# Optimization experiments

Measured on AMD Instinct MI355X. Metric: run time of the kernel, lower is better.

## Reference

```python
import jax, jax.numpy as jnp
import numpy as np

N_NODES = 50000

def setup_inputs() -> dict:
    key = jax.random.key(0)
    k1, k2, k3, k4, k5 = jax.random.split(key, 5)
    x = jax.random.normal(k1, (4, N_NODES, 128), dtype=jnp.float32)
    weights = jax.random.normal(k2, (128, 64), dtype=jnp.float32) * (np.sqrt(2.0) * np.sqrt(6.0 / (128 + 64)))
    edge_vals = jax.random.uniform(k3, (800000,), dtype=jnp.float32)
    edge_rows = jax.random.randint(k4, (800000,), 0, N_NODES, dtype=jnp.int32)
    edge_cols = jax.random.randint(k5, (800000,), 0, N_NODES, dtype=jnp.int32)
    return {"x": x, "weights": weights, "edge_vals": edge_vals,
            "edge_rows": edge_rows, "edge_cols": edge_cols}

def reference(x, weights, edge_vals, edge_rows, edge_cols):
    # x: [B, N, Din]; weights: [Din, Dout]; adj as COO edges (shared across batch)
    pre = jnp.einsum('bni,io->bno', x, weights)          # dense GEMM per sample
    msg = pre[:, edge_cols, :] * edge_vals[None, :, None]  # [B, E, Dout] gather+scale
    # sparse adj @ pre: scatter-add messages to destination rows, per batch sample
    agg = jax.vmap(lambda m: jax.ops.segment_sum(m, edge_rows, num_segments=N_NODES))(msg)
    return jax.nn.relu(agg)
```

## Files before the change

kernel.cpp:

```cpp
#include <hip/hip_runtime.h>
#include <hip/hip_bf16.h>


#define B_BATCH 4
#define DIN 128
#define DOUT 64
#define CAP 64

typedef float f32x4 __attribute__((ext_vector_type(4)));
typedef short s16x8 __attribute__((ext_vector_type(8)));

static __device__ __forceinline__ unsigned short f2bf(float f) {
  unsigned u = __builtin_bit_cast(unsigned, f);
  unsigned r = (u + 0x7fff + ((u >> 16) & 1)) >> 16;
  return (unsigned short)r;
}
static __device__ __forceinline__ float lo16(unsigned u) {
  return __builtin_bit_cast(float, u << 16);
}
static __device__ __forceinline__ float hi16(unsigned u) {
  return __builtin_bit_cast(float, u & 0xffff0000u);
}

__global__ __launch_bounds__(256) void prep_wfrag_zero_kernel(
    const float* __restrict__ w, uint4* __restrict__ wimg,
    int* __restrict__ cnt, int n) {
  const int t = threadIdx.x;
  if (blockIdx.x != 0) {
    int i = (blockIdx.x - 1) * 256 + t;
    if (i < n) cnt[i] = 0;
    return;
  }
  for (int i = 0; i < 8; ++i) {
    int idx = i * 256 + t;
    int fslot = idx >> 6;
    int lane = idx & 63;
    int term = fslot & 1;
    int cks = fslot >> 1;
    int ct = cks >> 2, ks = cks & 3;
    int nn = ct * 16 + (lane & 15);
    int kb = ks * 32 + 4 * ((lane >> 4) & 3);
    unsigned short e[8];
#pragma unroll
    for (int j = 0; j < 8; ++j) {
      int k = kb + 16 * (j >> 2) + (j & 3);
      float wv = w[k * DOUT + nn];
      unsigned ub = __builtin_bit_cast(unsigned, wv);
      unsigned hib = ub & 0xffff0000u;
      if (term == 0) {
        e[j] = (unsigned short)(hib >> 16);
      } else {
        float lof = wv - __builtin_bit_cast(float, hib);
        e[j] = (unsigned short)(__builtin_bit_cast(unsigned, lof) >> 16);
      }
    }
    uint4 q;
    q.x = (unsigned)e[0] | ((unsigned)e[1] << 16);
    q.y = (unsigned)e[2] | ((unsigned)e[3] << 16);
    q.z = (unsigned)e[4] | ((unsigned)e[5] << 16);
    q.w = (unsigned)e[6] | ((unsigned)e[7] << 16);
    wimg[idx] = q;
  }
}

__global__ __launch_bounds__(256) void gemm_fill_kernel(
    const float* __restrict__ x, const uint4* __restrict__ wimg,
    unsigned short* __restrict__ pre16, int N, int nWaveTiles,
    const int* __restrict__ erows, const int* __restrict__ ecols,
    const float* __restrict__ evals, int* __restrict__ cnt,
    int2* __restrict__ epk, int nE) {
  __shared__ uint4 wlds[2048];
  const int t = threadIdx.x;
  for (int i = t; i < 2048; i += 256) wlds[i] = wimg[i];
  __syncthreads();

  const int wtile = blockIdx.x * 4 + (t >> 6);
  if (wtile < nWaveTiles) {
    const int lane = t & 63;
    const int rowg = (lane >> 4) & 3;
    const int rloc = lane & 15;

    f32x4 acc[2][4];
#pragma unroll
    for (int rs = 0; rs < 2; ++rs)
#pragma unroll
      for (int ct = 0; ct < 4; ++ct) acc[rs][ct] = (f32x4){0.f, 0.f, 0.f, 0.f};

    const float* xb = x + (size_t)wtile * 32 * DIN;

#pragma unroll
    for (int ks = 0; ks < 4; ++ks) {
      s16x8 Ah[2], Al[2];
#pragma unroll
      for (int rs = 0; rs < 2; ++rs) {
        const float* xp = xb + (rs * 16 + rloc) * DIN + ks * 32 + 4 * rowg;
        float4 a0 = *(const float4*)xp;
        float4 a1 = *(const float4*)(xp + 16);

        unsigned b0 = __builtin_bit_cast(unsigned, a0.x);
        unsigned b1 = __builtin_bit_cast(unsigned, a0.y);
        unsigned b2 = __builtin_bit_cast(unsigned, a0.z);
        unsigned b3 = __builtin_bit_cast(unsigned, a0.w);
        unsigned c0 = __builtin_bit_cast(unsigned, a1.x);
        unsigned c1 = __builtin_bit_cast(unsigned, a1.y);
        unsigned c2 = __builtin_bit_cast(unsigned, a1.z);
        unsigned c3 = __builtin_bit_cast(unsigned, a1.w);

        union { s16x8 v; unsigned u[4]; } H, L;
        H.u[0] = (b0 >> 16) | (b1 & 0xffff0000u);
        H.u[1] = (b2 >> 16) | (b3 & 0xffff0000u);
        H.u[2] = (c0 >> 16) | (c1 & 0xffff0000u);
        H.u[3] = (c2 >> 16) | (c3 & 0xffff0000u);

        float l0 = a0.x - hi16(b0);
        float l1 = a0.y - hi16(b1);
        float l2 = a0.z - hi16(b2);
        float l3 = a0.w - hi16(b3);
        float l4 = a1.x - hi16(c0);
        float l5 = a1.y - hi16(c1);
        float l6 = a1.z - hi16(c2);
        float l7 = a1.w - hi16(c3);
        L.u[0] = (__builtin_bit_cast(unsigned, l0) >> 16) |
                 (__builtin_bit_cast(unsigned, l1) & 0xffff0000u);
        L.u[1] = (__builtin_bit_cast(unsigned, l2) >> 16) |
                 (__builtin_bit_cast(unsigned, l3) & 0xffff0000u);
        L.u[2] = (__builtin_bit_cast(unsigned, l4) >> 16) |
                 (__builtin_bit_cast(unsigned, l5) & 0xffff0000u);
        L.u[3] = (__builtin_bit_cast(unsigned, l6) >> 16) |
                 (__builtin_bit_cast(unsigned, l7) & 0xffff0000u);
        Ah[rs] = H.v;
        Al[rs] = L.v;
      }

#pragma unroll
      for (int ct = 0; ct < 4; ++ct) {
        const int fbase = (ct * 4 + ks) * 2;
        s16x8 Bh = *(const s16x8*)&wlds[fbase * 64 + lane];
        s16x8 Bl = *(const s16x8*)&wlds[(fbase + 1) * 64 + lane];
#pragma unroll
        for (int rs = 0; rs < 2; ++rs) {
          acc[rs][ct] = __builtin_amdgcn_mfma_f32_16x16x32_bf16(Ah[rs], Bh, acc[rs][ct], 0, 0, 0);
          acc[rs][ct] = __builtin_amdgcn_mfma_f32_16x16x32_bf16(Ah[rs], Bl, acc[rs][ct], 0, 0, 0);
          acc[rs][ct] = __builtin_amdgcn_mfma_f32_16x16x32_bf16(Al[rs], Bh, acc[rs][ct], 0, 0, 0);
        }
      }
    }

#pragma unroll
    for (int rs = 0; rs < 2; ++rs) {
#pragma unroll
      for (int r = 0; r < 4; ++r) {
        int m = wtile * 32 + rs * 16 + 4 * rowg + r;
        int b = m / N;
        int n = m - b * N;
        size_t o = (size_t)n * 256 + b * 64 + rloc;
#pragma unroll
        for (int ct = 0; ct < 4; ++ct) {
          pre16[o + ct * 16] = f2bf(acc[rs][ct][r]);
        }
      }
    }
  }

  const int stride = gridDim.x * 256;
  for (int e = blockIdx.x * 256 + t; e < nE; e += stride) {
    int r = erows[e];
    int slot = atomicAdd(&cnt[r], 1);
    if (slot < CAP)
      epk[r * CAP + slot] = make_int2(ecols[e], __builtin_bit_cast(int, evals[e]));
  }
}

__global__ __launch_bounds__(256) void gather_rows_kernel(
    const unsigned short* __restrict__ pre16, const int* __restrict__ cnt,
    const int2* __restrict__ epk, float* __restrict__ out, int N, int NS) {
  const int wid  = blockIdx.x * 4 + (threadIdx.x >> 6);
  const int lane = threadIdx.x & 63;
  if (wid >= N) return;

  const int m    = min(cnt[wid], CAP);
  const int eh   = lane >> 5;
  const int loff = ((lane >> 3) & 3) * 64 + (lane & 7) * 8;

  int   c = 0;
  float v = 0.0f;
  if (lane < m) {
    int2 r = epk[wid * CAP + lane];
    c = r.x;
    v = __builtin_bit_cast(float, r.y);
  }

  float a0 = 0.f, a1 = 0.f, a2 = 0.f, a3 = 0.f;
  float a4 = 0.f, a5 = 0.f, a6 = 0.f, a7 = 0.f;

  auto edge2 = [&](int j) {
    int   cj = __shfl(c, j + eh, 64);
    float vj = __shfl(v, j + eh, 64);
    const uint4 q = *(const uint4*)(pre16 + (size_t)cj * 256 + loff);
    a0 = fmaf(vj, lo16(q.x), a0);
    a1 = fmaf(vj, hi16(q.x), a1);
    a2 = fmaf(vj, lo16(q.y), a2);
    a3 = fmaf(vj, hi16(q.y), a3);
    a4 = fmaf(vj, lo16(q.z), a4);
    a5 = fmaf(vj, hi16(q.z), a5);
    a6 = fmaf(vj, lo16(q.w), a6);
    a7 = fmaf(vj, hi16(q.w), a7);
  };

  int j = 0;
  for (; j + 7 < m; j += 8) { edge2(j); edge2(j + 2); edge2(j + 4); edge2(j + 6); }
  for (; j + 1 < m; j += 2) { edge2(j); }
  if (j < m) {
    int   cj = __shfl(c, j, 64);
    float vj = __shfl(v, j, 64);
    if (eh) vj = 0.0f;
    const uint4 q = *(const uint4*)(pre16 + (size_t)cj * 256 + loff);
    a0 = fmaf(vj, lo16(q.x), a0);
    a1 = fmaf(vj, hi16(q.x), a1);
    a2 = fmaf(vj, lo16(q.y), a2);
    a3 = fmaf(vj, hi16(q.y), a3);
    a4 = fmaf(vj, lo16(q.z), a4);
    a5 = fmaf(vj, hi16(q.z), a5);
    a6 = fmaf(vj, lo16(q.w), a6);
    a7 = fmaf(vj, hi16(q.w), a7);
  }

  a0 += __shfl_xor(a0, 32, 64);
  a1 += __shfl_xor(a1, 32, 64);
  a2 += __shfl_xor(a2, 32, 64);
  a3 += __shfl_xor(a3, 32, 64);
  a4 += __shfl_xor(a4, 32, 64);
  a5 += __shfl_xor(a5, 32, 64);
  a6 += __shfl_xor(a6, 32, 64);
  a7 += __shfl_xor(a7, 32, 64);

  if (lane < 32) {
    const int b   = lane >> 3;
    const int ch8 = (lane & 7) * 8;
    size_t o = (size_t)b * NS + (size_t)wid * DOUT + ch8;
    *(float4*)&out[o]     = make_float4(fmaxf(a0, 0.f), fmaxf(a1, 0.f),
                                        fmaxf(a2, 0.f), fmaxf(a3, 0.f));
    *(float4*)&out[o + 4] = make_float4(fmaxf(a4, 0.f), fmaxf(a5, 0.f),
                                        fmaxf(a6, 0.f), fmaxf(a7, 0.f));
  }
}

extern "C" void kernel_launch(void* const* d_in, const int* in_sizes, int n_in,
                              void* d_out, int out_size, void* d_ws, size_t ws_size,
                              hipStream_t stream) {
  const float* x     = (const float*)d_in[0];
  const float* w     = (const float*)d_in[1];
  const float* evals = (const float*)d_in[2];
  const int*   erows = (const int*)d_in[3];
  const int*   ecols = (const int*)d_in[4];
  float* out = (float*)d_out;

  const int N  = in_sizes[0] / (B_BATCH * DIN);
  const int E  = in_sizes[2];
  const int M  = B_BATCH * N;
  const int NS = N * DOUT;
  const int nWaveTiles = M / 32;

  size_t off = 0;
  auto alloc = [&](size_t bytes) {
    size_t o = off;
    off += (bytes + 255) & ~(size_t)255;
    return o;
  };
  size_t pre_off  = alloc((size_t)M * DOUT * 2);
  size_t wimg_off = alloc((size_t)2048 * 16);
  size_t cnt_off  = alloc((size_t)N * 4);
  size_t epk_off  = alloc((size_t)N * CAP * 8);
  (void)ws_size;

  char* ws = (char*)d_ws;
  unsigned short* pre16 = (unsigned short*)(ws + pre_off);
  uint4* wimg = (uint4*)(ws + wimg_off);
  int*   cnt  = (int*)(ws + cnt_off);
  int2*  epk  = (int2*)(ws + epk_off);

  prep_wfrag_zero_kernel<<<1 + (N + 255) / 256, 256, 0, stream>>>(w, wimg, cnt, N);

  gemm_fill_kernel<<<(nWaveTiles + 3) / 4, 256, 0, stream>>>(
      x, wimg, pre16, N, nWaveTiles, erows, ecols, evals, cnt, epk, E);

  gather_rows_kernel<<<(N + 3) / 4, 256, 0, stream>>>(pre16, cnt, epk, out, N, NS);
}
```

Baseline: 130.4 us.

## Split edge bucketing out of GEMM kernel and prefetch next x k-slice

```diff
diff --git a/kernel.cpp b/kernel.cpp
--- a/kernel.cpp
+++ b/kernel.cpp
@@ -63,112 +63,128 @@
   }
 }
 
-__global__ __launch_bounds__(256) void gemm_fill_kernel(
+__global__ __launch_bounds__(256, 4) void gemm_mfma_kernel(
     const float* __restrict__ x, const uint4* __restrict__ wimg,
-    unsigned short* __restrict__ pre16, int N, int nWaveTiles,
-    const int* __restrict__ erows, const int* __restrict__ ecols,
-    const float* __restrict__ evals, int* __restrict__ cnt,
-    int2* __restrict__ epk, int nE) {
+    unsigned short* __restrict__ pre16, int N, int nWaveTiles) {
   __shared__ uint4 wlds[2048];
   const int t = threadIdx.x;
   for (int i = t; i < 2048; i += 256) wlds[i] = wimg[i];
   __syncthreads();
 
   const int wtile = blockIdx.x * 4 + (t >> 6);
-  if (wtile < nWaveTiles) {
-    const int lane = t & 63;
-    const int rowg = (lane >> 4) & 3;
-    const int rloc = lane & 15;
-
-    f32x4 acc[2][4];
-#pragma unroll
-    for (int rs = 0; rs < 2; ++rs)
-#pragma unroll
-      for (int ct = 0; ct < 4; ++ct) acc[rs][ct] = (f32x4){0.f, 0.f, 0.f, 0.f};
-
-    const float* xb = x + (size_t)wtile * 32 * DIN;
-
-#pragma unroll
-    for (int ks = 0; ks < 4; ++ks) {
-      s16x8 Ah[2], Al[2];
+  if (wtile >= nWaveTiles) return;
+  const int lane = t & 63;
+  const int rowg = (lane >> 4) & 3;
+  const int rloc = lane & 15;
+
+  f32x4 acc[2][4];
+#pragma unroll
+  for (int rs = 0; rs < 2; ++rs)
+#pragma unroll
+    for (int ct = 0; ct < 4; ++ct) acc[rs][ct] = (f32x4){0.f, 0.f, 0.f, 0.f};
+
+  const float* xp0 = x + (size_t)wtile * 32 * DIN + rloc * DIN + 4 * rowg;
+  const float* xp1 = xp0 + 16 * DIN;
+
+  float4 ca0 = *(const float4*)(xp0);
+  float4 cb0 = *(const float4*)(xp0 + 16);
+  float4 ca1 = *(const float4*)(xp1);
+  float4 cb1 = *(const float4*)(xp1 + 16);
+
+#pragma unroll
+  for (int ks = 0; ks < 4; ++ks) {
+    float4 na0, nb0, na1, nb1;
+    if (ks < 3) {
+      const int d = (ks + 1) * 32;
+      na0 = *(const float4*)(xp0 + d);
+      nb0 = *(const float4*)(xp0 + d + 16);
+      na1 = *(const float4*)(xp1 + d);
+      nb1 = *(const float4*)(xp1 + d + 16);
+    }
+
+    s16x8 Ah[2], Al[2];
+#pragma unroll
+    for (int rs = 0; rs < 2; ++rs) {
+      float4 a0 = rs ? ca1 : ca0;
+      float4 a1 = rs ? cb1 : cb0;
+
+      unsigned b0 = __builtin_bit_cast(unsigned, a0.x);
+      unsigned b1 = __builtin_bit_cast(unsigned, a0.y);
+      unsigned b2 = __builtin_bit_cast(unsigned, a0.z);
+      unsigned b3 = __builtin_bit_cast(unsigned, a0.w);
+      unsigned c0 = __builtin_bit_cast(unsigned, a1.x);
+      unsigned c1 = __builtin_bit_cast(unsigned, a1.y);
+      unsigned c2 = __builtin_bit_cast(unsigned, a1.z);
+      unsigned c3 = __builtin_bit_cast(unsigned, a1.w);
+
+      union { s16x8 v; unsigned u[4]; } H, L;
+      H.u[0] = (b0 >> 16) | (b1 & 0xffff0000u);
+      H.u[1] = (b2 >> 16) | (b3 & 0xffff0000u);
+      H.u[2] = (c0 >> 16) | (c1 & 0xffff0000u);
+      H.u[3] = (c2 >> 16) | (c3 & 0xffff0000u);
+
+      float l0 = a0.x - hi16(b0);
+      float l1 = a0.y - hi16(b1);
+      float l2 = a0.z - hi16(b2);
+      float l3 = a0.w - hi16(b3);
+      float l4 = a1.x - hi16(c0);
+      float l5 = a1.y - hi16(c1);
+      float l6 = a1.z - hi16(c2);
+      float l7 = a1.w - hi16(c3);
+      L.u[0] = (__builtin_bit_cast(unsigned, l0) >> 16) |
+               (__builtin_bit_cast(unsigned, l1) & 0xffff0000u);
+      L.u[1] = (__builtin_bit_cast(unsigned, l2) >> 16) |
+               (__builtin_bit_cast(unsigned, l3) & 0xffff0000u);
+      L.u[2] = (__builtin_bit_cast(unsigned, l4) >> 16) |
+               (__builtin_bit_cast(unsigned, l5) & 0xffff0000u);
+      L.u[3] = (__builtin_bit_cast(unsigned, l6) >> 16) |
+               (__builtin_bit_cast(unsigned, l7) & 0xffff0000u);
+      Ah[rs] = H.v;
+      Al[rs] = L.v;
+    }
+
+#pragma unroll
+    for (int ct = 0; ct < 4; ++ct) {
+      const int fbase = (ct * 4 + ks) * 2;
+      s16x8 Bh = *(const s16x8*)&wlds[fbase * 64 + lane];
+      s16x8 Bl = *(const s16x8*)&wlds[(fbase + 1) * 64 + lane];
 #pragma unroll
       for (int rs = 0; rs < 2; ++rs) {
-        const float* xp = xb + (rs * 16 + rloc) * DIN + ks * 32 + 4 * rowg;
-        float4 a0 = *(const float4*)xp;
-        float4 a1 = *(const float4*)(xp + 16);
-
-        unsigned b0 = __builtin_bit_cast(unsigned, a0.x);
-        unsigned b1 = __builtin_bit_cast(unsigned, a0.y);
-        unsigned b2 = __builtin_bit_cast(unsigned, a0.z);
-        unsigned b3 = __builtin_bit_cast(unsigned, a0.w);
-        unsigned c0 = __builtin_bit_cast(unsigned, a1.x);
-        unsigned c1 = __builtin_bit_cast(unsigned, a1.y);
-        unsigned c2 = __builtin_bit_cast(unsigned, a1.z);
-        unsigned c3 = __builtin_bit_cast(unsigned, a1.w);
-
-        union { s16x8 v; unsigned u[4]; } H, L;
-        H.u[0] = (b0 >> 16) | (b1 & 0xffff0000u);
-        H.u[1] = (b2 >> 16) | (b3 & 0xffff0000u);
-        H.u[2] = (c0 >> 16) | (c1 & 0xffff0000u);
-        H.u[3] = (c2 >> 16) | (c3 & 0xffff0000u);
-
-        float l0 = a0.x - hi16(b0);
-        float l1 = a0.y - hi16(b1);
-        float l2 = a0.z - hi16(b2);
-        float l3 = a0.w - hi16(b3);
-        float l4 = a1.x - hi16(c0);
-        float l5 = a1.y - hi16(c1);
-        float l6 = a1.z - hi16(c2);
-        float l7 = a1.w - hi16(c3);
-        L.u[0] = (__builtin_bit_cast(unsigned, l0) >> 16) |
-                 (__builtin_bit_cast(unsigned, l1) & 0xffff0000u);
-        L.u[1] = (__builtin_bit_cast(unsigned, l2) >> 16) |
-                 (__builtin_bit_cast(unsigned, l3) & 0xffff0000u);
-        L.u[2] = (__builtin_bit_cast(unsigned, l4) >> 16) |
-                 (__builtin_bit_cast(unsigned, l5) & 0xffff0000u);
-        L.u[3] = (__builtin_bit_cast(unsigned, l6) >> 16) |
-                 (__builtin_bit_cast(unsigned, l7) & 0xffff0000u);
-        Ah[rs] = H.v;
-        Al[rs] = L.v;
+        acc[rs][ct] = __builtin_amdgcn_mfma_f32_16x16x32_bf16(Ah[rs], Bh, acc[rs][ct], 0, 0, 0);
+        acc[rs][ct] = __builtin_amdgcn_mfma_f32_16x16x32_bf16(Ah[rs], Bl, acc[rs][ct], 0, 0, 0);
+        acc[rs][ct] = __builtin_amdgcn_mfma_f32_16x16x32_bf16(Al[rs], Bh, acc[rs][ct], 0, 0, 0);
       }
-
+    }
+
+    if (ks < 3) { ca0 = na0; cb0 = nb0; ca1 = na1; cb1 = nb1; }
+  }
+
+#pragma unroll
+  for (int rs = 0; rs < 2; ++rs) {
+#pragma unroll
+    for (int r = 0; r < 4; ++r) {
+      int m = wtile * 32 + rs * 16 + 4 * rowg + r;
+      int b = m / N;
+      int n = m - b * N;
+      size_t o = (size_t)n * 256 + b * 64 + rloc;
 #pragma unroll
       for (int ct = 0; ct < 4; ++ct) {
-        const int fbase = (ct * 4 + ks) * 2;
-        s16x8 Bh = *(const s16x8*)&wlds[fbase * 64 + lane];
-        s16x8 Bl = *(const s16x8*)&wlds[(fbase + 1) * 64 + lane];
-#pragma unroll
-        for (int rs = 0; rs < 2; ++rs) {
-          acc[rs][ct] = __builtin_amdgcn_mfma_f32_16x16x32_bf16(Ah[rs], Bh, acc[rs][ct], 0, 0, 0);
-          acc[rs][ct] = __builtin_amdgcn_mfma_f32_16x16x32_bf16(Ah[rs], Bl, acc[rs][ct], 0, 0, 0);
-          acc[rs][ct] = __builtin_amdgcn_mfma_f32_16x16x32_bf16(Al[rs], Bh, acc[rs][ct], 0, 0, 0);
-        }
+        pre16[o + ct * 16] = f2bf(acc[rs][ct][r]);
       }
     }
-
-#pragma unroll
-    for (int rs = 0; rs < 2; ++rs) {
-#pragma unroll
-      for (int r = 0; r < 4; ++r) {
-        int m = wtile * 32 + rs * 16 + 4 * rowg + r;
-        int b = m / N;
-        int n = m - b * N;
-        size_t o = (size_t)n * 256 + b * 64 + rloc;
-#pragma unroll
-        for (int ct = 0; ct < 4; ++ct) {
-          pre16[o + ct * 16] = f2bf(acc[rs][ct][r]);
-        }
-      }
-    }
-  }
-
-  const int stride = gridDim.x * 256;
-  for (int e = blockIdx.x * 256 + t; e < nE; e += stride) {
-    int r = erows[e];
-    int slot = atomicAdd(&cnt[r], 1);
-    if (slot < CAP)
-      epk[r * CAP + slot] = make_int2(ecols[e], __builtin_bit_cast(int, evals[e]));
-  }
+  }
+}
+
+__global__ __launch_bounds__(256) void fill_kernel(
+    const int* __restrict__ erows, const int* __restrict__ ecols,
+    const float* __restrict__ evals, int* __restrict__ cnt,
+    int2* __restrict__ epk, int nE) {
+  int e = blockIdx.x * 256 + threadIdx.x;
+  if (e >= nE) return;
+  int r = erows[e];
+  int slot = atomicAdd(&cnt[r], 1);
+  if (slot < CAP)
+    epk[r * CAP + slot] = make_int2(ecols[e], __builtin_bit_cast(int, evals[e]));
 }
 
 __global__ __launch_bounds__(256) void gather_rows_kernel(
@@ -281,8 +297,9 @@
 
   prep_wfrag_zero_kernel<<<1 + (N + 255) / 256, 256, 0, stream>>>(w, wimg, cnt, N);
 
-  gemm_fill_kernel<<<(nWaveTiles + 3) / 4, 256, 0, stream>>>(
-      x, wimg, pre16, N, nWaveTiles, erows, ecols, evals, cnt, epk, E);
+  gemm_mfma_kernel<<<(nWaveTiles + 3) / 4, 256, 0, stream>>>(x, wimg, pre16, N, nWaveTiles);
+
+  fill_kernel<<<(E + 255) / 256, 256, 0, stream>>>(erows, ecols, evals, cnt, epk, E);
 
   gather_rows_kernel<<<(N + 3) / 4, 256, 0, stream>>>(pre16, cnt, epk, out, N, NS);
 }
```

After: 140.3 us. 7.6% more time.
